# Optimization experiments

Measured on AMD Instinct MI355X. Metric: run time of the kernel, lower is better.

The kernel has to match this reference:

```python
import jax, jax.numpy as jnp
import numpy as np

B, M, K = 4096, 64, 3          # graphs, points per graph, knn k
FX, FP = 59, 3                 # node features, position dims (FX+FP = 62)
EPS = 1e-5


def _lin_init(key, fan_in, fan_out):
    k1, k2 = jax.random.split(key)
    s = 1.0 / np.sqrt(fan_in)
    W = jax.random.uniform(k1, (fan_in, fan_out), jnp.float32, -s, s)
    b = jax.random.uniform(k2, (fan_out,), jnp.float32, -s, s)
    return W, b


def setup_inputs() -> dict:
    key = jax.random.key(0)
    ks = jax.random.split(key, 8)
    x = jax.random.normal(ks[0], (B * M, FX), jnp.float32)
    pos = jax.random.normal(ks[1], (B * M, FP), jnp.float32)
    batch = jnp.repeat(jnp.arange(B, dtype=jnp.int32), M)
    W1, b1 = _lin_init(ks[2], FX + FP, 128)
    W2, b2 = _lin_init(ks[3], 128, 128)
    Wc1, bc1 = _lin_init(ks[4], 128, 256)
    Wc2, bc2 = _lin_init(ks[5], 256, 1)
    return dict(
        x=x, pos=pos, batch=batch,
        W1=W1, b1=b1, g1=jnp.ones(128), be1=jnp.zeros(128),
        W2=W2, b2=b2, g2=jnp.ones(128), be2=jnp.zeros(128),
        Wc1=Wc1, bc1=bc1, gc1=jnp.ones(256), bec1=jnp.zeros(256),
        Wc2=Wc2, bc2=bc2, gc2=jnp.ones(1), bec2=jnp.zeros(1),
    )


def _mlp_block(h, W, b, g, be):
    # Linear -> ReLU -> BatchNorm1d (training-mode batch statistics)
    h = jax.nn.relu(h @ W + b)
    mu = h.mean(axis=0)
    var = h.var(axis=0)  # biased, as torch BN uses for normalization
    return g * (h - mu) * jax.lax.rsqrt(var + EPS) + be


def _knn_idx(pos_b):
    # pos_b: [B, M, FP]; per-graph k-NN (loop=False)
    d = jnp.sum((pos_b[:, :, None, :] - pos_b[:, None, :, :]) ** 2, axis=-1)  # [B,M,M]
    d = d + jnp.eye(M, dtype=d.dtype) * 1e10  # exclude self-loops
    _, nbr = jax.lax.top_k(-d, K)  # [B, M, K] neighbor (source) indices
    return nbr


def reference(x, pos, batch, W1, b1, g1, be1, W2, b2, g2, be2,
              Wc1, bc1, gc1, bec1, Wc2, bc2, gc2, bec2):
    x_b = x.reshape(B, M, FX)
    pos_b = pos.reshape(B, M, FP)
    nbr = _knn_idx(pos_b)                                   # [B,M,K]
    # gather neighbor features and relative positions (edge messages)
    xj = jax.vmap(lambda xb, nb: xb[nb])(x_b, nbr)          # [B,M,K,FX]
    pj = jax.vmap(lambda pb, nb: pb[nb])(pos_b, nbr)        # [B,M,K,FP]
    rel = pj - pos_b[:, :, None, :]
    msg = jnp.concatenate([xj, rel], axis=-1).reshape(B * M * K, FX + FP)
    # local_nn on every edge, then max aggregation per target node
    h = _mlp_block(msg, W1, b1, g1, be1)                    # [E,128]
    h = h.reshape(B, M, K, 128).max(axis=2).reshape(B * M, 128)
    # global_nn per node
    h = _mlp_block(h, W2, b2, g2, be2)                      # [N,128]
    # global mean pool over graphs
    sums = jax.ops.segment_sum(h, batch, num_segments=B)
    cnt = jax.ops.segment_sum(jnp.ones((B * M,), h.dtype), batch, num_segments=B)
    pooled = sums / cnt[:, None]                            # [B,128]
    # classifier MLP([128,256,1])
    c = _mlp_block(pooled, Wc1, bc1, gc1, bec1)
    c = _mlp_block(c, Wc2, bc2, gc2, bec2)                  # [B,1]
    return jax.nn.sigmoid(c)[:, 0]
```

## Files before the change

kernel.cpp:

```cpp
#include <hip/hip_runtime.h>
#include <hip/hip_bf16.h>
#include <math.h>

#define NB   4096
#define MM   64
#define KNN  3
#define FX   59
#define H    128
#define NN   (NB*MM)
#define NE   (NN*KNN)
#define C1   256
#define EPSB 1e-5f

typedef __attribute__((ext_vector_type(8))) short short8;
typedef __attribute__((ext_vector_type(4))) float f32x4;

__device__ __forceinline__ float wave_red(float v) {
#pragma unroll
    for (int m = 32; m >= 1; m >>= 1) v += __shfl_xor(v, m, 64);
    return v;
}

__device__ __forceinline__ unsigned short f2bf(float f) {
    union { float f; unsigned u; } v; v.f = f;
    unsigned r = v.u + 0x7fffu + ((v.u >> 16) & 1u);
    return (unsigned short)(r >> 16);
}

__device__ __forceinline__ unsigned int pack_bf2(float a, float b) {
    union { __hip_bfloat162 h; unsigned int u; } cv;
    cv.h = __float22bfloat162_rn(make_float2(a, b));
    return cv.u;
}

__global__ __launch_bounds__(64) void k_prep1(
    const float* __restrict__ W1, unsigned short* __restrict__ W1t)
{
    const int n = blockIdx.x, k = threadIdx.x;
    W1t[n * 64 + k] = (k < 62) ? f2bf(W1[k * H + n]) : (unsigned short)0;
}

__global__ __launch_bounds__(128) void k_prep2(
    const float* __restrict__ W2, const float* __restrict__ affine1,
    const float* __restrict__ b2, unsigned short* __restrict__ W2t,
    float* __restrict__ b2p)
{
    const int n = blockIdx.x, k = threadIdx.x;
    float wv = W2[k * H + n];
    W2t[n * H + k] = f2bf(affine1[k] * wv);
    float contrib = wave_red(affine1[H + k] * wv);
    __shared__ float red2[2];
    if ((k & 63) == 0) red2[k >> 6] = contrib;
    __syncthreads();
    if (k == 0) b2p[n] = b2[n] + red2[0] + red2[1];
}

__global__ __launch_bounds__(256) void k_knn_mfma1(
    const float* __restrict__ x, const float* __restrict__ pos,
    const unsigned short* __restrict__ W1t, const float* __restrict__ W1,
    const float* __restrict__ b1,
    unsigned short* __restrict__ h1max, float* __restrict__ p1s,
    float* __restrict__ p1q)
{
    __shared__ float pos_s[MM * 3];
    __shared__ int   nbr_s[MM * 3];
    __shared__ float b1_s[H];
    __shared__ float w1p_s[3 * H];
    __shared__ __align__(16) unsigned short a_s[MM * 72];
    __shared__ __align__(16) unsigned int   u_s32[MM * 66];

    const int blk = blockIdx.x, tid = threadIdx.x;
    const float* xg = x + (size_t)blk * MM * FX;
    const float* pg = pos + (size_t)blk * MM * 3;

    {
        const int node = tid >> 2, c0g = (tid & 3) * 16;
        unsigned short vals[16];
#pragma unroll
        for (int i = 0; i < 16; ++i) {
            int c = c0g + i;
            float v = (c < FX) ? xg[node * FX + c]
                               : ((c < 62) ? pg[node * 3 + (c - FX)] : 0.f);
            vals[i] = f2bf(v);
        }
        *(short8*)(a_s + node * 72 + c0g)     = *(short8*)&vals[0];
        *(short8*)(a_s + node * 72 + c0g + 8) = *(short8*)&vals[8];
    }
    for (int t = tid; t < MM * 3; t += 256) pos_s[t] = pg[t];
    if (tid < H) b1_s[tid] = b1[tid];
    for (int t = tid; t < 3 * H; t += 256) w1p_s[t] = W1[(FX + (t >> 7)) * H + (t & 127)];
    __syncthreads();

    {
        const int node = tid >> 2, q = tid & 3;
        const float px = pos_s[node * 3 + 0];
        const float py = pos_s[node * 3 + 1];
        const float pz = pos_s[node * 3 + 2];
        float d0 = 1e30f, d1 = 1e30f, d2 = 1e30f;
        int   i0 = 1 << 30, i1 = 1 << 30, i2 = 1 << 30;
        for (int jj = 0; jj < 16; ++jj) {
            int j = q * 16 + jj;
            if (j == node) continue;
            float dx = pos_s[j * 3 + 0] - px;
            float dy = pos_s[j * 3 + 1] - py;
            float dz = pos_s[j * 3 + 2] - pz;
            float d = dx * dx + dy * dy + dz * dz;
            bool b2v = (d < d2) || (d == d2 && j < i2);
            bool b1v = (d < d1) || (d == d1 && j < i1);
            bool b0v = (d < d0) || (d == d0 && j < i0);
            float nd2 = b1v ? d1 : d; int ni2 = b1v ? i1 : j;
            float nd1 = b0v ? d0 : d; int ni1 = b0v ? i0 : j;
            d2 = b2v ? nd2 : d2; i2 = b2v ? ni2 : i2;
            d1 = b1v ? nd1 : d1; i1 = b1v ? ni1 : i1;
            d0 = b0v ? d   : d0; i0 = b0v ? j   : i0;
        }
#pragma unroll
        for (int mq = 1; mq <= 2; mq <<= 1) {
            float e[3]; int f[3];
            e[0] = __shfl_xor(d0, mq, 64); f[0] = __shfl_xor(i0, mq, 64);
            e[1] = __shfl_xor(d1, mq, 64); f[1] = __shfl_xor(i1, mq, 64);
            e[2] = __shfl_xor(d2, mq, 64); f[2] = __shfl_xor(i2, mq, 64);
#pragma unroll
            for (int t3 = 0; t3 < 3; ++t3) {
                float ev = e[t3]; int fv = f[t3];
                bool b2v = (ev < d2) || (ev == d2 && fv < i2);
                bool b1v = (ev < d1) || (ev == d1 && fv < i1);
                bool b0v = (ev < d0) || (ev == d0 && fv < i0);
                float nd2 = b1v ? d1 : ev; int ni2 = b1v ? i1 : fv;
                float nd1 = b0v ? d0 : ev; int ni1 = b0v ? i0 : fv;
                d2 = b2v ? nd2 : d2; i2 = b2v ? ni2 : i2;
                d1 = b1v ? nd1 : d1; i1 = b1v ? ni1 : i1;
                d0 = b0v ? ev  : d0; i0 = b0v ? fv  : i0;
            }
        }
        if (q == 0) {
            nbr_s[node * 3 + 0] = i0;
            nbr_s[node * 3 + 1] = i1;
            nbr_s[node * 3 + 2] = i2;
        }
    }

    const int lane = tid & 63;
    const int w    = tid >> 6;
    const int wcol = w * 32;
    const int m    = lane & 15;
    const int kg   = lane >> 4;

    short8 bfr[2][2];
#pragma unroll
    for (int ct = 0; ct < 2; ++ct)
#pragma unroll
        for (int kc = 0; kc < 2; ++kc)
            bfr[ct][kc] = *(const short8*)(W1t + (wcol + ct * 16 + m) * 64 + kc * 32 + kg * 8);

    f32x4 acc[4][2];
#pragma unroll
    for (int rt = 0; rt < 4; ++rt)
#pragma unroll
        for (int ct = 0; ct < 2; ++ct) acc[rt][ct] = (f32x4){0.f, 0.f, 0.f, 0.f};

#pragma unroll
    for (int kc = 0; kc < 2; ++kc)
#pragma unroll
        for (int rt = 0; rt < 4; ++rt) {
            short8 a = *(const short8*)(a_s + (rt * 16 + m) * 72 + kc * 32 + kg * 8);
#pragma unroll
            for (int ct = 0; ct < 2; ++ct)
                acc[rt][ct] = __builtin_amdgcn_mfma_f32_16x16x32_bf16(bfr[ct][kc], a, acc[rt][ct], 0, 0, 0);
        }
#pragma unroll
    for (int rt = 0; rt < 4; ++rt)
#pragma unroll
        for (int ct = 0; ct < 2; ++ct) {
            int node = rt * 16 + m;
            int pidx = 16 * w + 8 * ct + 2 * kg;
            uint2 val;
            val.x = pack_bf2(acc[rt][ct][0], acc[rt][ct][1]);
            val.y = pack_bf2(acc[rt][ct][2], acc[rt][ct][3]);
            *(uint2*)(u_s32 + node * 66 + pidx) = val;
        }
    __syncthreads();

    const int c0 = 2 * lane, c1v = 2 * lane + 1;
    const float wpa0 = w1p_s[c0],      wpa1 = w1p_s[H + c0],  wpa2 = w1p_s[2 * H + c0];
    const float wpb0 = w1p_s[c1v],     wpb1 = w1p_s[H + c1v], wpb2 = w1p_s[2 * H + c1v];
    const float b1a = b1_s[c0], b1b = b1_s[c1v];
    float s0 = 0.f, s1 = 0.f, q0 = 0.f, q1 = 0.f;
    unsigned int* hout32 = (unsigned int*)(h1max + (size_t)blk * MM * H);
    for (int ii = 0; ii < 16; ++ii) {
        int node = w * 16 + ii;
        int j0 = nbr_s[node * 3 + 0];
        int j1 = nbr_s[node * 3 + 1];
        int j2 = nbr_s[node * 3 + 2];
        float px = pos_s[node * 3 + 0], py = pos_s[node * 3 + 1], pz = pos_s[node * 3 + 2];
        float basea = b1a - (px * wpa0 + py * wpa1 + pz * wpa2);
        float baseb = b1b - (px * wpb0 + py * wpb1 + pz * wpb2);
        unsigned int v0 = u_s32[j0 * 66 + lane];
        unsigned int v1 = u_s32[j1 * 66 + lane];
        unsigned int v2 = u_s32[j2 * 66 + lane];
        float h0a = fmaxf(__uint_as_float(v0 << 16) + basea, 0.f);
        float h1a = fmaxf(__uint_as_float(v1 << 16) + basea, 0.f);
        float h2a = fmaxf(__uint_as_float(v2 << 16) + basea, 0.f);
        float h0b = fmaxf(__uint_as_float(v0 & 0xffff0000u) + baseb, 0.f);
        float h1b = fmaxf(__uint_as_float(v1 & 0xffff0000u) + baseb, 0.f);
        float h2b = fmaxf(__uint_as_float(v2 & 0xffff0000u) + baseb, 0.f);
        s0 += h0a + h1a + h2a; q0 += h0a * h0a + h1a * h1a + h2a * h2a;
        s1 += h0b + h1b + h2b; q1 += h0b * h0b + h1b * h1b + h2b * h2b;
        float ma = fmaxf(fmaxf(h0a, h1a), h2a);
        float mb = fmaxf(fmaxf(h0b, h1b), h2b);
        hout32[node * 64 + lane] = pack_bf2(ma, mb);
    }

    float* red_s = (float*)a_s;
    *(float2*)(red_s + w * 128 + c0)       = make_float2(s0, s1);
    *(float2*)(red_s + 512 + w * 128 + c0) = make_float2(q0, q1);
    __syncthreads();
    if (tid < 128) {
        float S = red_s[tid] + red_s[128 + tid] + red_s[256 + tid] + red_s[384 + tid];
        p1s[(size_t)blk * H + tid] = S;
    } else {
        int t2 = tid - 128;
        float Q = red_s[512 + t2] + red_s[640 + t2] + red_s[768 + t2] + red_s[896 + t2];
        p1q[(size_t)blk * H + t2] = Q;
    }
}

__global__ __launch_bounds__(256) void k_stats(
    const float* __restrict__ ps, const float* __restrict__ pq, int P, int ld,
    float invCnt, const float* __restrict__ g, const float* __restrict__ be,
    float* __restrict__ affine, int C)
{
    const int c = blockIdx.x, tid = threadIdx.x;
    float s = 0.f, q = 0.f;
    for (int p = tid; p < P; p += 256) {
        s += ps[(size_t)p * ld + c];
        q += pq[(size_t)p * ld + c];
    }
    s = wave_red(s); q = wave_red(q);
    __shared__ float rs_s[4], rq_s[4];
    if ((tid & 63) == 0) { rs_s[tid >> 6] = s; rq_s[tid >> 6] = q; }
    __syncthreads();
    if (tid == 0) {
        float S = rs_s[0] + rs_s[1] + rs_s[2] + rs_s[3];
        float Q = rq_s[0] + rq_s[1] + rq_s[2] + rq_s[3];
        float mu  = S * invCnt;
        float var = Q * invCnt - mu * mu;
        float a   = g[c] * rsqrtf(var + EPSB);
        affine[c]     = a;
        affine[C + c] = be[c] - mu * a;
    }
}

__global__ __launch_bounds__(256) void k_mfma2(
    const unsigned short* __restrict__ h1max, const unsigned short* __restrict__ W2t,
    const float* __restrict__ b2p,
    float* __restrict__ graphsum, float* __restrict__ p2s, float* __restrict__ p2q)
{
    __shared__ __align__(16) unsigned short a_s[MM * 136];
    const int blk = blockIdx.x, tid = threadIdx.x;
    const unsigned short* hg = h1max + (size_t)blk * MM * H;
    for (int t = tid; t < MM * H / 8; t += 256) {
        int row = t >> 4, col8 = (t & 15) * 8;
        *(short8*)(a_s + row * 136 + col8) = *(const short8*)(hg + row * H + col8);
    }
    __syncthreads();

    const int lane = tid & 63, w = tid >> 6, wcol = w * 32;
    const int m = lane & 15, kg = lane >> 4;

    short8 bfr[2][4];
#pragma unroll
    for (int ct = 0; ct < 2; ++ct)
#pragma unroll
        for (int kc = 0; kc < 4; ++kc)
            bfr[ct][kc] = *(const short8*)(W2t + (wcol + ct * 16 + m) * H + kc * 32 + kg * 8);

    f32x4 acc[4][2];
#pragma unroll
    for (int rt = 0; rt < 4; ++rt)
#pragma unroll
        for (int ct = 0; ct < 2; ++ct) acc[rt][ct] = (f32x4){0.f, 0.f, 0.f, 0.f};

#pragma unroll
    for (int kc = 0; kc < 4; ++kc)
#pragma unroll
        for (int rt = 0; rt < 4; ++rt) {
            short8 a = *(const short8*)(a_s + (rt * 16 + m) * 136 + kc * 32 + kg * 8);
#pragma unroll
            for (int ct = 0; ct < 2; ++ct)
                acc[rt][ct] = __builtin_amdgcn_mfma_f32_16x16x32_bf16(a, bfr[ct][kc], acc[rt][ct], 0, 0, 0);
        }

#pragma unroll
    for (int ct = 0; ct < 2; ++ct) {
        float bv = b2p[wcol + ct * 16 + m];
        float s = 0.f, q = 0.f;
#pragma unroll
        for (int rt = 0; rt < 4; ++rt)
#pragma unroll
            for (int r = 0; r < 4; ++r) {
                float v = fmaxf(acc[rt][ct][r] + bv, 0.f);
                s += v; q += v * v;
            }
        s += __shfl_xor(s, 16, 64); q += __shfl_xor(q, 16, 64);
        s += __shfl_xor(s, 32, 64); q += __shfl_xor(q, 32, 64);
        if (lane < 16) {
            int col = wcol + ct * 16 + lane;
            graphsum[(size_t)blk * H + col] = s;
            p2s[(size_t)blk * H + col] = s;
            p2q[(size_t)blk * H + col] = q;
        }
    }
}

__global__ __launch_bounds__(256) void k_cls1(
    const float* __restrict__ graphsum, const float* __restrict__ affine2,
    const float* __restrict__ Wc1, const float* __restrict__ bc1,
    float* __restrict__ c1raw, float* __restrict__ p3s, float* __restrict__ p3q)
{
    __shared__ float pooled_s[16 * H];
    const int blk = blockIdx.x, tid = threadIdx.x;
    const int g0 = blk * 16;
    for (int t = tid; t < 16 * H; t += 256) {
        int f = t & 127;
        pooled_s[t] = affine2[f] * (graphsum[(size_t)g0 * H + t] * (1.f / 64.f)) + affine2[H + f];
    }
    __syncthreads();
    const int c = tid;
    float acc[16];
    const float bias = bc1[c];
#pragma unroll
    for (int gi = 0; gi < 16; ++gi) acc[gi] = bias;
    for (int f = 0; f < H; ++f) {
        float w = Wc1[f * C1 + c];
#pragma unroll
        for (int gi = 0; gi < 16; ++gi) acc[gi] += pooled_s[gi * H + f] * w;
    }
    float s = 0.f, q = 0.f;
#pragma unroll
    for (int gi = 0; gi < 16; ++gi) {
        float h = fmaxf(acc[gi], 0.f);
        c1raw[(size_t)(g0 + gi) * C1 + c] = h;
        s += h; q += h * h;
    }
    p3s[(size_t)blk * C1 + c] = s;
    p3q[(size_t)blk * C1 + c] = q;
}

__global__ __launch_bounds__(256) void k_cls2(
    const float* __restrict__ c1raw, const float* __restrict__ affine3,
    const float* __restrict__ Wc2, const float* __restrict__ bc2,
    float* __restrict__ z, float* __restrict__ pz, float* __restrict__ pzq)
{
    __shared__ float a_s[C1], c_s[C1], w_s[C1];
    const int blk = blockIdx.x, tid = threadIdx.x;
    a_s[tid] = affine3[tid];
    c_s[tid] = affine3[C1 + tid];
    w_s[tid] = Wc2[tid];
    __syncthreads();
    const int g = blk * 256 + tid;
    float acc = bc2[0];
    for (int f = 0; f < C1; f += 4) {
        float4 cv = *(const float4*)&c1raw[(size_t)g * C1 + f];
        acc += (a_s[f + 0] * cv.x + c_s[f + 0]) * w_s[f + 0];
        acc += (a_s[f + 1] * cv.y + c_s[f + 1]) * w_s[f + 1];
        acc += (a_s[f + 2] * cv.z + c_s[f + 2]) * w_s[f + 2];
        acc += (a_s[f + 3] * cv.w + c_s[f + 3]) * w_s[f + 3];
    }
    float zz = fmaxf(acc, 0.f);
    z[g] = zz;
    float s = wave_red(zz);
    float q = wave_red(zz * zz);
    __shared__ float rs_s[4], rq_s[4];
    if ((tid & 63) == 0) { rs_s[tid >> 6] = s; rq_s[tid >> 6] = q; }
    __syncthreads();
    if (tid == 0) {
        pz[blk]  = rs_s[0] + rs_s[1] + rs_s[2] + rs_s[3];
        pzq[blk] = rq_s[0] + rq_s[1] + rq_s[2] + rq_s[3];
    }
}

__global__ __launch_bounds__(256) void k_final(
    const float* __restrict__ z, const float* __restrict__ pz,
    const float* __restrict__ pzq, const float* __restrict__ gc2,
    const float* __restrict__ bec2, float* __restrict__ out)
{
    __shared__ float ab[2];
    if (threadIdx.x == 0) {
        float S = 0.f, Q = 0.f;
        for (int p = 0; p < 16; ++p) { S += pz[p]; Q += pzq[p]; }
        float mu  = S * (1.f / 4096.f);
        float var = Q * (1.f / 4096.f) - mu * mu;
        float a   = gc2[0] * rsqrtf(var + EPSB);
        ab[0] = a;
        ab[1] = bec2[0] - mu * a;
    }
    __syncthreads();
    float a = ab[0], cb = ab[1];
    for (int g = threadIdx.x; g < NB; g += 256) {
        float v = a * z[g] + cb;
        out[g] = 1.f / (1.f + expf(-v));
    }
}

extern "C" void kernel_launch(void* const* d_in, const int* in_sizes, int n_in,
                              void* d_out, int out_size, void* d_ws, size_t ws_size,
                              hipStream_t stream)
{
    const float* x    = (const float*)d_in[0];
    const float* pos  = (const float*)d_in[1];
    const float* W1   = (const float*)d_in[3];
    const float* b1   = (const float*)d_in[4];
    const float* g1   = (const float*)d_in[5];
    const float* be1  = (const float*)d_in[6];
    const float* W2   = (const float*)d_in[7];
    const float* b2   = (const float*)d_in[8];
    const float* g2   = (const float*)d_in[9];
    const float* be2  = (const float*)d_in[10];
    const float* Wc1  = (const float*)d_in[11];
    const float* bc1  = (const float*)d_in[12];
    const float* gc1  = (const float*)d_in[13];
    const float* bec1 = (const float*)d_in[14];
    const float* Wc2  = (const float*)d_in[15];
    const float* bc2  = (const float*)d_in[16];
    const float* gc2  = (const float*)d_in[17];
    const float* bec2 = (const float*)d_in[18];
    float* out = (float*)d_out;

    float* ws = (float*)d_ws;
    size_t off = 0;
    auto alloc = [&](size_t n) { float* p = ws + off; off += n; return p; };
    unsigned short* h1max = (unsigned short*)alloc((size_t)NN * H / 2);
    unsigned short* W1t   = (unsigned short*)alloc(128 * 64 / 2);
    unsigned short* W2t   = (unsigned short*)alloc(128 * 128 / 2);
    float* b2p     = alloc(H);
    float* p1s     = alloc((size_t)NB * H);
    float* p1q     = alloc((size_t)NB * H);
    float* affine1 = alloc(2 * H);
    float* graphsum= alloc((size_t)NB * H);
    float* p2s     = alloc((size_t)NB * H);
    float* p2q     = alloc((size_t)NB * H);
    float* affine2 = alloc(2 * H);
    float* c1raw   = alloc((size_t)NB * C1);
    float* p3s     = alloc((size_t)256 * C1);
    float* p3q     = alloc((size_t)256 * C1);
    float* affine3 = alloc(2 * C1);
    float* zbuf    = alloc(NB);
    float* pz      = alloc(16);
    float* pzq     = alloc(16);

    k_prep1<<<dim3(128), dim3(64), 0, stream>>>(W1, W1t);
    k_knn_mfma1<<<dim3(NB), dim3(256), 0, stream>>>(x, pos, W1t, W1, b1, h1max, p1s, p1q);
    k_stats<<<dim3(H), dim3(256), 0, stream>>>(p1s, p1q, NB, H, 1.f / (float)NE, g1, be1, affine1, H);
    k_prep2<<<dim3(128), dim3(128), 0, stream>>>(W2, affine1, b2, W2t, b2p);
    k_mfma2<<<dim3(NB), dim3(256), 0, stream>>>(h1max, W2t, b2p, graphsum, p2s, p2q);
    k_stats<<<dim3(H), dim3(256), 0, stream>>>(p2s, p2q, NB, H, 1.f / (float)NN, g2, be2, affine2, H);
    k_cls1<<<dim3(256), dim3(256), 0, stream>>>(graphsum, affine2, Wc1, bc1, c1raw, p3s, p3q);
    k_stats<<<dim3(C1), dim3(256), 0, stream>>>(p3s, p3q, 256, C1, 1.f / (float)NB, gc1, bec1, affine3, C1);
    k_cls2<<<dim3(16), dim3(256), 0, stream>>>(c1raw, affine3, Wc2, bc2, zbuf, pz, pzq);
    k_final<<<dim3(1), dim3(256), 0, stream>>>(zbuf, pz, pzq, gc2, bec2, out);
}
```

Baseline: 260.4 us.

## Widen kNN/MFMA1 blocks to 512 threads, fold W1 prep, drop duplicate buffers

The fused kNN plus first-layer kernel now runs 512 threads per graph, so each wave computes 16 output channels and each node's neighbor search is split across 8 lanes instead of 4. The separate W1 transpose/convert kernel is removed, and each block converts its W1 fragment inline from fp32, adding redundant global loads per block. The second MFMA kernel reads A fragments straight from global memory instead of staging them in LDS. The redundant p2s buffer is dropped and graphsum is passed to the stats kernel in its place.

```diff
diff --git a/kernel.cpp b/kernel.cpp
--- a/kernel.cpp
+++ b/kernel.cpp
@@ -33,13 +33,6 @@
     return cv.u;
 }
 
-__global__ __launch_bounds__(64) void k_prep1(
-    const float* __restrict__ W1, unsigned short* __restrict__ W1t)
-{
-    const int n = blockIdx.x, k = threadIdx.x;
-    W1t[n * 64 + k] = (k < 62) ? f2bf(W1[k * H + n]) : (unsigned short)0;
-}
-
 __global__ __launch_bounds__(128) void k_prep2(
     const float* __restrict__ W2, const float* __restrict__ affine1,
     const float* __restrict__ b2, unsigned short* __restrict__ W2t,
@@ -55,10 +48,9 @@
     if (k == 0) b2p[n] = b2[n] + red2[0] + red2[1];
 }
 
-__global__ __launch_bounds__(256) void k_knn_mfma1(
+__global__ __launch_bounds__(512, 8) void k_knn_mfma1(
     const float* __restrict__ x, const float* __restrict__ pos,
-    const unsigned short* __restrict__ W1t, const float* __restrict__ W1,
-    const float* __restrict__ b1,
+    const float* __restrict__ W1, const float* __restrict__ b1,
     unsigned short* __restrict__ h1max, float* __restrict__ p1s,
     float* __restrict__ p1q)
 {
@@ -74,32 +66,49 @@
     const float* pg = pos + (size_t)blk * MM * 3;
 
     {
-        const int node = tid >> 2, c0g = (tid & 3) * 16;
-        unsigned short vals[16];
-#pragma unroll
-        for (int i = 0; i < 16; ++i) {
+        const int node = tid >> 3, c0g = (tid & 7) * 8;
+        unsigned short vals[8];
+#pragma unroll
+        for (int i = 0; i < 8; ++i) {
             int c = c0g + i;
             float v = (c < FX) ? xg[node * FX + c]
                                : ((c < 62) ? pg[node * 3 + (c - FX)] : 0.f);
             vals[i] = f2bf(v);
         }
-        *(short8*)(a_s + node * 72 + c0g)     = *(short8*)&vals[0];
-        *(short8*)(a_s + node * 72 + c0g + 8) = *(short8*)&vals[8];
-    }
-    for (int t = tid; t < MM * 3; t += 256) pos_s[t] = pg[t];
+        *(short8*)(a_s + node * 72 + c0g) = *(short8*)&vals[0];
+    }
+    if (tid < MM * 3) pos_s[tid] = pg[tid];
     if (tid < H) b1_s[tid] = b1[tid];
-    for (int t = tid; t < 3 * H; t += 256) w1p_s[t] = W1[(FX + (t >> 7)) * H + (t & 127)];
+    if (tid < 3 * H) w1p_s[tid] = W1[(FX + (tid >> 7)) * H + (tid & 127)];
+
+    const int lane = tid & 63;
+    const int w    = tid >> 6;
+    const int m    = lane & 15;
+    const int kg   = lane >> 4;
+    const int ch   = w * 16 + m;
+
+    short8 bfr[2];
+#pragma unroll
+    for (int kc = 0; kc < 2; ++kc) {
+        unsigned short t8[8];
+#pragma unroll
+        for (int i = 0; i < 8; ++i) {
+            int k = kc * 32 + kg * 8 + i;
+            t8[i] = (k < 62) ? f2bf(W1[k * H + ch]) : (unsigned short)0;
+        }
+        bfr[kc] = *(short8*)t8;
+    }
     __syncthreads();
 
     {
-        const int node = tid >> 2, q = tid & 3;
+        const int node = tid >> 3, q = tid & 7;
         const float px = pos_s[node * 3 + 0];
         const float py = pos_s[node * 3 + 1];
         const float pz = pos_s[node * 3 + 2];
         float d0 = 1e30f, d1 = 1e30f, d2 = 1e30f;
         int   i0 = 1 << 30, i1 = 1 << 30, i2 = 1 << 30;
-        for (int jj = 0; jj < 16; ++jj) {
-            int j = q * 16 + jj;
+        for (int jj = 0; jj < 8; ++jj) {
+            int j = q * 8 + jj;
             if (j == node) continue;
             float dx = pos_s[j * 3 + 0] - px;
             float dy = pos_s[j * 3 + 1] - py;
@@ -115,7 +124,7 @@
             d0 = b0v ? d   : d0; i0 = b0v ? j   : i0;
         }
 #pragma unroll
-        for (int mq = 1; mq <= 2; mq <<= 1) {
+        for (int mq = 1; mq <= 4; mq <<= 1) {
             float e[3]; int f[3];
             e[0] = __shfl_xor(d0, mq, 64); f[0] = __shfl_xor(i0, mq, 64);
             e[1] = __shfl_xor(d1, mq, 64); f[1] = __shfl_xor(i1, mq, 64);
@@ -140,45 +149,26 @@
         }
     }
 
-    const int lane = tid & 63;
-    const int w    = tid >> 6;
-    const int wcol = w * 32;
-    const int m    = lane & 15;
-    const int kg   = lane >> 4;
-
-    short8 bfr[2][2];
-#pragma unroll
-    for (int ct = 0; ct < 2; ++ct)
-#pragma unroll
-        for (int kc = 0; kc < 2; ++kc)
-            bfr[ct][kc] = *(const short8*)(W1t + (wcol + ct * 16 + m) * 64 + kc * 32 + kg * 8);
-
-    f32x4 acc[4][2];
-#pragma unroll
-    for (int rt = 0; rt < 4; ++rt)
-#pragma unroll
-        for (int ct = 0; ct < 2; ++ct) acc[rt][ct] = (f32x4){0.f, 0.f, 0.f, 0.f};
+    f32x4 acc[4];
+#pragma unroll
+    for (int rt = 0; rt < 4; ++rt) acc[rt] = (f32x4){0.f, 0.f, 0.f, 0.f};
 
 #pragma unroll
     for (int kc = 0; kc < 2; ++kc)
 #pragma unroll
         for (int rt = 0; rt < 4; ++rt) {
             short8 a = *(const short8*)(a_s + (rt * 16 + m) * 72 + kc * 32 + kg * 8);
-#pragma unroll
-            for (int ct = 0; ct < 2; ++ct)
-                acc[rt][ct] = __builtin_amdgcn_mfma_f32_16x16x32_bf16(bfr[ct][kc], a, acc[rt][ct], 0, 0, 0);
-        }
-#pragma unroll
-    for (int rt = 0; rt < 4; ++rt)
-#pragma unroll
-        for (int ct = 0; ct < 2; ++ct) {
-            int node = rt * 16 + m;
-            int pidx = 16 * w + 8 * ct + 2 * kg;
-            uint2 val;
-            val.x = pack_bf2(acc[rt][ct][0], acc[rt][ct][1]);
-            val.y = pack_bf2(acc[rt][ct][2], acc[rt][ct][3]);
-            *(uint2*)(u_s32 + node * 66 + pidx) = val;
-        }
+            acc[rt] = __builtin_amdgcn_mfma_f32_16x16x32_bf16(bfr[kc], a, acc[rt], 0, 0, 0);
+        }
+#pragma unroll
+    for (int rt = 0; rt < 4; ++rt) {
+        int node = rt * 16 + m;
+        int pidx = 8 * w + 2 * kg;
+        uint2 val;
+        val.x = pack_bf2(acc[rt][0], acc[rt][1]);
+        val.y = pack_bf2(acc[rt][2], acc[rt][3]);
+        *(uint2*)(u_s32 + node * 66 + pidx) = val;
+    }
     __syncthreads();
 
     const int c0 = 2 * lane, c1v = 2 * lane + 1;
@@ -187,8 +177,9 @@
     const float b1a = b1_s[c0], b1b = b1_s[c1v];
     float s0 = 0.f, s1 = 0.f, q0 = 0.f, q1 = 0.f;
     unsigned int* hout32 = (unsigned int*)(h1max + (size_t)blk * MM * H);
-    for (int ii = 0; ii < 16; ++ii) {
-        int node = w * 16 + ii;
+#pragma unroll
+    for (int ii = 0; ii < 8; ++ii) {
+        int node = w * 8 + ii;
         int j0 = nbr_s[node * 3 + 0];
         int j1 = nbr_s[node * 3 + 1];
         int j2 = nbr_s[node * 3 + 2];
@@ -210,17 +201,23 @@
         float mb = fmaxf(fmaxf(h0b, h1b), h2b);
         hout32[node * 64 + lane] = pack_bf2(ma, mb);
     }
-
-    float* red_s = (float*)a_s;
-    *(float2*)(red_s + w * 128 + c0)       = make_float2(s0, s1);
-    *(float2*)(red_s + 512 + w * 128 + c0) = make_float2(q0, q1);
+    __syncthreads();
+
+    float* s_red = (float*)a_s;
+    float* q_red = (float*)u_s32;
+    *(float2*)(s_red + w * 128 + c0) = make_float2(s0, s1);
+    *(float2*)(q_red + w * 128 + c0) = make_float2(q0, q1);
     __syncthreads();
     if (tid < 128) {
-        float S = red_s[tid] + red_s[128 + tid] + red_s[256 + tid] + red_s[384 + tid];
+        float S = 0.f;
+#pragma unroll
+        for (int ww = 0; ww < 8; ++ww) S += s_red[ww * 128 + tid];
         p1s[(size_t)blk * H + tid] = S;
-    } else {
+    } else if (tid < 256) {
         int t2 = tid - 128;
-        float Q = red_s[512 + t2] + red_s[640 + t2] + red_s[768 + t2] + red_s[896 + t2];
+        float Q = 0.f;
+#pragma unroll
+        for (int ww = 0; ww < 8; ++ww) Q += q_red[ww * 128 + t2];
         p1q[(size_t)blk * H + t2] = Q;
     }
 }
@@ -254,17 +251,10 @@
 __global__ __launch_bounds__(256) void k_mfma2(
     const unsigned short* __restrict__ h1max, const unsigned short* __restrict__ W2t,
     const float* __restrict__ b2p,
-    float* __restrict__ graphsum, float* __restrict__ p2s, float* __restrict__ p2q)
-{
-    __shared__ __align__(16) unsigned short a_s[MM * 136];
+    float* __restrict__ graphsum, float* __restrict__ p2q)
+{
     const int blk = blockIdx.x, tid = threadIdx.x;
     const unsigned short* hg = h1max + (size_t)blk * MM * H;
-    for (int t = tid; t < MM * H / 8; t += 256) {
-        int row = t >> 4, col8 = (t & 15) * 8;
-        *(short8*)(a_s + row * 136 + col8) = *(const short8*)(hg + row * H + col8);
-    }
-    __syncthreads();
-
     const int lane = tid & 63, w = tid >> 6, wcol = w * 32;
     const int m = lane & 15, kg = lane >> 4;
 
@@ -285,7 +275,7 @@
     for (int kc = 0; kc < 4; ++kc)
 #pragma unroll
         for (int rt = 0; rt < 4; ++rt) {
-            short8 a = *(const short8*)(a_s + (rt * 16 + m) * 136 + kc * 32 + kg * 8);
+            short8 a = *(const short8*)(hg + (rt * 16 + m) * H + kc * 32 + kg * 8);
 #pragma unroll
             for (int ct = 0; ct < 2; ++ct)
                 acc[rt][ct] = __builtin_amdgcn_mfma_f32_16x16x32_bf16(a, bfr[ct][kc], acc[rt][ct], 0, 0, 0);
@@ -307,7 +297,6 @@
         if (lane < 16) {
             int col = wcol + ct * 16 + lane;
             graphsum[(size_t)blk * H + col] = s;
-            p2s[(size_t)blk * H + col] = s;
             p2q[(size_t)blk * H + col] = q;
         }
     }
@@ -431,14 +420,12 @@
     size_t off = 0;
     auto alloc = [&](size_t n) { float* p = ws + off; off += n; return p; };
     unsigned short* h1max = (unsigned short*)alloc((size_t)NN * H / 2);
-    unsigned short* W1t   = (unsigned short*)alloc(128 * 64 / 2);
     unsigned short* W2t   = (unsigned short*)alloc(128 * 128 / 2);
     float* b2p     = alloc(H);
     float* p1s     = alloc((size_t)NB * H);
     float* p1q     = alloc((size_t)NB * H);
     float* affine1 = alloc(2 * H);
     float* graphsum= alloc((size_t)NB * H);
-    float* p2s     = alloc((size_t)NB * H);
     float* p2q     = alloc((size_t)NB * H);
     float* affine2 = alloc(2 * H);
     float* c1raw   = alloc((size_t)NB * C1);
@@ -449,12 +436,11 @@
     float* pz      = alloc(16);
     float* pzq     = alloc(16);
 
-    k_prep1<<<dim3(128), dim3(64), 0, stream>>>(W1, W1t);
-    k_knn_mfma1<<<dim3(NB), dim3(256), 0, stream>>>(x, pos, W1t, W1, b1, h1max, p1s, p1q);
+    k_knn_mfma1<<<dim3(NB), dim3(512), 0, stream>>>(x, pos, W1, b1, h1max, p1s, p1q);
     k_stats<<<dim3(H), dim3(256), 0, stream>>>(p1s, p1q, NB, H, 1.f / (float)NE, g1, be1, affine1, H);
     k_prep2<<<dim3(128), dim3(128), 0, stream>>>(W2, affine1, b2, W2t, b2p);
-    k_mfma2<<<dim3(NB), dim3(256), 0, stream>>>(h1max, W2t, b2p, graphsum, p2s, p2q);
-    k_stats<<<dim3(H), dim3(256), 0, stream>>>(p2s, p2q, NB, H, 1.f / (float)NN, g2, be2, affine2, H);
+    k_mfma2<<<dim3(NB), dim3(256), 0, stream>>>(h1max, W2t, b2p, graphsum, p2q);
+    k_stats<<<dim3(H), dim3(256), 0, stream>>>(graphsum, p2q, NB, H, 1.f / (float)NN, g2, be2, affine2, H);
     k_cls1<<<dim3(256), dim3(256), 0, stream>>>(graphsum, affine2, Wc1, bc1, c1raw, p3s, p3q);
     k_stats<<<dim3(C1), dim3(256), 0, stream>>>(p3s, p3q, 256, C1, 1.f / (float)NB, gc1, bec1, affine3, C1);
     k_cls2<<<dim3(16), dim3(256), 0, stream>>>(c1raw, affine3, Wc2, bc2, zbuf, pz, pzq);
```

Measured after the change: 278.9 us. +7.1%, slower.
